# Kernel optimization log

Measured on AMD Instinct MI355X. Metric: run time of the kernel, lower is better.

Reference implementation:

```python
import jax, jax.numpy as jnp
import numpy as np

T, B, DIM_IN, DIM_STATE, NUM_CLASSES = 256, 64, 256, 512, 10000


def setup_inputs() -> dict:
    key = jax.random.key(0)
    ks = jax.random.split(key, 6)
    inputs = jax.random.normal(ks[0], (T, B, DIM_IN), dtype=jnp.float32)
    labels = jax.random.uniform(ks[1], (T, B, NUM_CLASSES), dtype=jnp.float32)
    labels = labels / jnp.sum(labels, axis=-1, keepdims=True)  # soft label distributions
    initial_state = jnp.zeros((B, DIM_STATE), dtype=jnp.float32)
    initial_output = jnp.zeros((B, DIM_STATE), dtype=jnp.float32)
    # LSTM cell params: gates packed as [i, f, g, o]
    Wx = jax.random.normal(ks[2], (DIM_IN, 4 * DIM_STATE), dtype=jnp.float32) * (1.0 / np.sqrt(DIM_IN))
    Wh = jax.random.normal(ks[3], (DIM_STATE, 4 * DIM_STATE), dtype=jnp.float32) * (1.0 / np.sqrt(DIM_STATE))
    b = jnp.zeros((4 * DIM_STATE,), dtype=jnp.float32)
    # Final FC (softmax head) params
    Wo = jax.random.normal(ks[4], (DIM_STATE, NUM_CLASSES), dtype=jnp.float32) * (1.0 / np.sqrt(DIM_STATE))
    bo = jnp.zeros((NUM_CLASSES,), dtype=jnp.float32)
    return {"inputs": inputs, "labels": labels, "initial_state": initial_state,
            "initial_output": initial_output, "Wx": Wx, "Wh": Wh, "b": b, "Wo": Wo, "bo": bo}


def reference(inputs, labels, initial_state, initial_output, Wx, Wh, b, Wo, bo):
    def step(carry, x_t):
        h, c = carry  # h: [B, DIM_STATE] previous output; c: [B, DIM_STATE] cell state
        z = x_t @ Wx + h @ Wh + b  # [B, 4*DIM_STATE]
        i, f, g, o = jnp.split(z, 4, axis=-1)
        c = jax.nn.sigmoid(f) * c + jax.nn.sigmoid(i) * jnp.tanh(g)
        h = jax.nn.sigmoid(o) * jnp.tanh(c)
        return (h, c), h

    _, hs = jax.lax.scan(step, (initial_output, initial_state), inputs)  # hs: [T, B, DIM_STATE]
    logits = jnp.einsum('tbs,sc->tbc', hs, Wo) + bo  # [T, B, NUM_CLASSES]
    log_p = jax.nn.log_softmax(logits, axis=-1)
    predictions = jnp.exp(log_p)  # softmax probabilities
    # softmax_cross_entropy_with_logits per (t, b), then mean over all
    total_loss = -jnp.mean(jnp.sum(labels * log_p, axis=-1))
    return predictions, total_loss
```

## Files before the change

kernel.cpp:

```cpp
#include <hip/hip_runtime.h>
#include <hip/hip_bf16.h>
#include <math.h>

#define T_STEPS 256
#define BATCH 64
#define DIN 256
#define DSTATE 512
#define NGATE 2048
#define NCLS 10000
#define NCLS_PAD 10112
#define ROWS 16384
#define SCAN_BLOCKS 64
#define GROUP_BLOCKS 16
#define CHUNK_ROWS 4096

typedef __attribute__((ext_vector_type(8))) short bf16x8;
typedef __attribute__((ext_vector_type(4))) float f32x4;

__device__ inline unsigned short f2b(float x) {
    __hip_bfloat16 h = __float2bfloat16(x);
    return *(unsigned short*)&h;
}
__device__ inline float b2f(unsigned short u) {
    return __uint_as_float(((unsigned int)u) << 16);
}

__launch_bounds__(256)
__global__ void prep_all(const float* __restrict__ inputs, const float* __restrict__ Wx,
                         const float* __restrict__ Wh, const float* __restrict__ bias,
                         const float* __restrict__ h0, const float* __restrict__ Wo,
                         unsigned short* __restrict__ Xb, unsigned short* __restrict__ WxT,
                         unsigned short* __restrict__ WhT, float* __restrict__ bp,
                         unsigned short* __restrict__ h0b, unsigned* __restrict__ bar,
                         unsigned short* __restrict__ WoT) {
    __shared__ float tile[64][65];
    const int bid = blockIdx.x;
    const int tid = threadIdx.x;
    if (bid < 4096) {
        int i = bid * 256 + tid;
        float4 v = *(const float4*)&inputs[(size_t)i * 4];
        ushort4 o; o.x = f2b(v.x); o.y = f2b(v.y); o.z = f2b(v.z); o.w = f2b(v.w);
        *(ushort4*)&Xb[(size_t)i * 4] = o;
    } else if (bid < 8192) {
        int e = (bid - 4096) * 256 + tid;
        int jp = e >> 9, k = e & 511;
        int s = jp >> 2, g = jp & 3;
        WhT[e] = f2b(Wh[(size_t)k * NGATE + g * DSTATE + s]);
    } else if (bid < 10240) {
        int e = (bid - 8192) * 256 + tid;
        int jp = e >> 8, k = e & 255;
        int s = jp >> 2, g = jp & 3;
        WxT[e] = f2b(Wx[(size_t)k * NGATE + g * DSTATE + s]);
    } else if (bid < 10248) {
        int jp = (bid - 10240) * 256 + tid;
        if (jp < NGATE) bp[jp] = bias[(jp & 3) * DSTATE + (jp >> 2)];
    } else if (bid < 10280) {
        int i = (bid - 10248) * 256 + tid;
        if (i < BATCH * DSTATE / 4) {
            float4 v = *(const float4*)&h0[(size_t)i * 4];
            ushort4 o; o.x = f2b(v.x); o.y = f2b(v.y); o.z = f2b(v.z); o.w = f2b(v.w);
            *(ushort4*)&h0b[(size_t)i * 4] = o;
        }
    } else if (bid < 10284) {
        bar[(bid - 10280) * 256 + tid] = 0u;
    } else {
        int nb = bid - 10284;
        int n0 = (nb % 158) * 64, k0 = (nb / 158) * 64;
        #pragma unroll
        for (int r = 0; r < 16; ++r) {
            int k = (tid >> 6) + r * 4;
            int n = tid & 63;
            float v = (n0 + n < NCLS) ? Wo[(size_t)(k0 + k) * NCLS + n0 + n] : 0.f;
            tile[k][n] = v;
        }
        __syncthreads();
        #pragma unroll
        for (int r = 0; r < 16; ++r) {
            int n = (tid >> 6) + r * 4;
            int k = tid & 63;
            WoT[(size_t)(n0 + n) * DSTATE + k0 + k] = f2b(tile[k][n]);
        }
    }
}

__launch_bounds__(256)
__global__ void zx_gemm(const unsigned short* __restrict__ Xb,
                        const unsigned short* __restrict__ WxT,
                        const float* __restrict__ bp,
                        unsigned short* __restrict__ ZxT) {
    __shared__ unsigned short As[64][264];
    __shared__ unsigned short Bs[128][264];
    __shared__ float zls[4][32][65];
    const int tid = threadIdx.x;
    const int t = blockIdx.x;
    const int n0 = blockIdx.y * 128;
    const int wave = tid >> 6, lane = tid & 63, mr = lane & 15, g = lane >> 4;

    #pragma unroll
    for (int r = 0; r < 8; ++r) {
        int c = r * 256 + tid; int row = c >> 5, q = c & 31;
        *(int4*)&As[row][q * 8] = *(const int4*)&Xb[((size_t)t * 64 + row) * DIN + q * 8];
    }
    #pragma unroll
    for (int r = 0; r < 16; ++r) {
        int c = r * 256 + tid; int row = c >> 5, q = c & 31;
        *(int4*)&Bs[row][q * 8] = *(const int4*)&WxT[(size_t)(n0 + row) * DIN + q * 8];
    }
    __syncthreads();

    f32x4 acc[4][2] = {};
    #pragma unroll
    for (int kt = 0; kt < DIN; kt += 32) {
        bf16x8 af[4], bf[2];
        #pragma unroll
        for (int fm = 0; fm < 4; ++fm) af[fm] = *(const bf16x8*)&As[fm * 16 + mr][kt + g * 8];
        #pragma unroll
        for (int fn = 0; fn < 2; ++fn) bf[fn] = *(const bf16x8*)&Bs[wave * 32 + fn * 16 + mr][kt + g * 8];
        #pragma unroll
        for (int fm = 0; fm < 4; ++fm)
            #pragma unroll
            for (int fn = 0; fn < 2; ++fn)
                acc[fm][fn] = __builtin_amdgcn_mfma_f32_16x16x32_bf16(af[fm], bf[fn], acc[fm][fn], 0, 0, 0);
    }
    #pragma unroll
    for (int fm = 0; fm < 4; ++fm)
        #pragma unroll
        for (int fn = 0; fn < 2; ++fn)
            #pragma unroll
            for (int r = 0; r < 4; ++r)
                zls[wave][fn * 16 + mr][fm * 16 + g * 4 + r] = acc[fm][fn][r];
    #pragma unroll 4
    for (int jr = 0; jr < 32; ++jr) {
        int j = n0 + wave * 32 + jr;
        float v = zls[wave][jr][lane] + bp[j];
        ZxT[((size_t)t * NGATE + j) * 64 + lane] = f2b(v);
    }
}

__device__ __forceinline__ void groupbar(unsigned* fbase, int w, unsigned want, int tid) {
    __syncthreads();
    if (tid == 0)
        __hip_atomic_store(&fbase[w * 16], want, __ATOMIC_RELEASE, __HIP_MEMORY_SCOPE_AGENT);
    if (tid < GROUP_BLOCKS) {
        while (__hip_atomic_load(&fbase[tid * 16], __ATOMIC_RELAXED, __HIP_MEMORY_SCOPE_AGENT) < want) {}
        (void)__hip_atomic_load(&fbase[tid * 16], __ATOMIC_ACQUIRE, __HIP_MEMORY_SCOPE_AGENT);
    }
    __syncthreads();
}

__launch_bounds__(256, 1)
__global__ void lstm_scan_mfma(const unsigned short* __restrict__ h0b,
                               const float* __restrict__ c0,
                               const unsigned short* __restrict__ WhT,
                               const unsigned short* __restrict__ ZxT,
                               unsigned short* __restrict__ hsb,
                               unsigned* __restrict__ bar) {
    __shared__ unsigned short Wl[128][520];
    __shared__ unsigned short hT[16][520];
    __shared__ float zb[16][132];
    const int tid = threadIdx.x;
    const int bid = blockIdx.x;
    const int grp = bid >> 4;
    const int w   = bid & 15;
    const int b0  = grp * 16;
    const int j0  = w * 128;
    const int s0  = w * 32;
    const int wave = tid >> 6, lane = tid & 63, mr = lane & 15, gl = lane >> 4;
    unsigned* fbase = bar + grp * 256;

    #pragma unroll 4
    for (int r = 0; r < 32; ++r) {
        int c = r * 256 + tid; int row = c >> 6, q = c & 63;
        *(int4*)&Wl[row][q * 8] = *(const int4*)&WhT[(size_t)(j0 + row) * DSTATE + q * 8];
    }

    const int gb  = lane >> 2;
    const int slg = wave * 8 + (lane & 3) * 2;
    float creg0 = c0[(b0 + gb) * DSTATE + s0 + slg];
    float creg1 = c0[(b0 + gb) * DSTATE + s0 + slg + 1];
    __syncthreads();

    const size_t zo0 = ((size_t)(j0 + wave * 32 + mr)) * 64 + b0 + gl * 4;
    const size_t zo1 = ((size_t)(j0 + wave * 32 + 16 + mr)) * 64 + b0 + gl * 4;
    ushort4 za0 = *(const ushort4*)&ZxT[zo0];
    ushort4 za1 = *(const ushort4*)&ZxT[zo1];

    for (int t = 0; t < T_STEPS; ++t) {
        const unsigned short* hsrc = t ? (hsb + (size_t)(t - 1) * BATCH * DSTATE) : h0b;
        #pragma unroll
        for (int r = 0; r < 4; ++r) {
            int c = r * 256 + tid; int row = c >> 6, q = c & 63;
            *(int4*)&hT[row][q * 8] = *(const int4*)&hsrc[(size_t)(b0 + row) * DSTATE + q * 8];
        }
        __syncthreads();

        f32x4 acc0, acc1;
        acc0[0] = b2f(za0.x); acc0[1] = b2f(za0.y); acc0[2] = b2f(za0.z); acc0[3] = b2f(za0.w);
        acc1[0] = b2f(za1.x); acc1[1] = b2f(za1.y); acc1[2] = b2f(za1.z); acc1[3] = b2f(za1.w);
        if (t + 1 < T_STEPS) {
            za0 = *(const ushort4*)&ZxT[(size_t)(t + 1) * NGATE * 64 + zo0];
            za1 = *(const ushort4*)&ZxT[(size_t)(t + 1) * NGATE * 64 + zo1];
        }
        #pragma unroll
        for (int kt = 0; kt < DSTATE; kt += 32) {
            bf16x8 af = *(const bf16x8*)&hT[mr][kt + gl * 8];
            acc0 = __builtin_amdgcn_mfma_f32_16x16x32_bf16(af, *(const bf16x8*)&Wl[wave * 32 + mr][kt + gl * 8], acc0, 0, 0, 0);
            acc1 = __builtin_amdgcn_mfma_f32_16x16x32_bf16(af, *(const bf16x8*)&Wl[wave * 32 + 16 + mr][kt + gl * 8], acc1, 0, 0, 0);
        }
        #pragma unroll
        for (int r = 0; r < 4; ++r) {
            zb[gl * 4 + r][wave * 32 + mr] = acc0[r];
            zb[gl * 4 + r][wave * 32 + 16 + mr] = acc1[r];
        }
        {
            float zi0 = zb[gb][slg * 4 + 0], zf0 = zb[gb][slg * 4 + 1];
            float zg0 = zb[gb][slg * 4 + 2], zo0v = zb[gb][slg * 4 + 3];
            float zi1 = zb[gb][slg * 4 + 4], zf1 = zb[gb][slg * 4 + 5];
            float zg1 = zb[gb][slg * 4 + 6], zo1v = zb[gb][slg * 4 + 7];
            float i0 = 1.f / (1.f + expf(-zi0)), f0 = 1.f / (1.f + expf(-zf0));
            float o0 = 1.f / (1.f + expf(-zo0v)), g0 = tanhf(zg0);
            float i1 = 1.f / (1.f + expf(-zi1)), f1 = 1.f / (1.f + expf(-zf1));
            float o1 = 1.f / (1.f + expf(-zo1v)), g1 = tanhf(zg1);
            creg0 = f0 * creg0 + i0 * g0;
            creg1 = f1 * creg1 + i1 * g1;
            float h0v = o0 * tanhf(creg0);
            float h1v = o1 * tanhf(creg1);
            ushort2 hv; hv.x = f2b(h0v); hv.y = f2b(h1v);
            *(ushort2*)&hsb[((size_t)t * BATCH + b0 + gb) * DSTATE + s0 + slg] = hv;
        }
        if (t != T_STEPS - 1)
            groupbar(fbase, w, (unsigned)(t + 1), tid);
    }
}

__launch_bounds__(256)
__global__ void gemm_logits_bf16(const unsigned short* __restrict__ A,
                                 const unsigned short* __restrict__ Bt,
                                 const float* __restrict__ bo,
                                 unsigned short* __restrict__ Cb) {
    __shared__ unsigned short As[128 * 32];
    __shared__ unsigned short Bs[128 * 32];
    __shared__ unsigned short sC[128][136];
    const int tid = threadIdx.x;
    const int wave = tid >> 6, lane = tid & 63;
    const int wm = wave >> 1, wn = wave & 1;
    const int m0 = blockIdx.y * 128, n0 = blockIdx.x * 128;
    const int g = lane >> 4, mr = lane & 15;

    const int ch0 = wave * 64 + lane;
    const int ch1 = (4 + wave) * 64 + lane;
    const int row0 = ch0 >> 2, q0 = ch0 & 3;
    const int row1 = ch1 >> 2, q1 = ch1 & 3;

    f32x4 acc[4][4] = {};
    for (int kt = 0; kt < DSTATE; kt += 32) {
        __builtin_amdgcn_global_load_lds(
            (const __attribute__((address_space(1))) void*)&A[(size_t)(m0 + row0) * DSTATE + kt + q0 * 8],
            (__attribute__((address_space(3))) void*)&As[ch0 * 8 - lane * 8], 16, 0, 0);
        __builtin_amdgcn_global_load_lds(
            (const __attribute__((address_space(1))) void*)&A[(size_t)(m0 + row1) * DSTATE + kt + q1 * 8],
            (__attribute__((address_space(3))) void*)&As[ch1 * 8 - lane * 8], 16, 0, 0);
        __builtin_amdgcn_global_load_lds(
            (const __attribute__((address_space(1))) void*)&Bt[(size_t)(n0 + row0) * DSTATE + kt + q0 * 8],
            (__attribute__((address_space(3))) void*)&Bs[ch0 * 8 - lane * 8], 16, 0, 0);
        __builtin_amdgcn_global_load_lds(
            (const __attribute__((address_space(1))) void*)&Bt[(size_t)(n0 + row1) * DSTATE + kt + q1 * 8],
            (__attribute__((address_space(3))) void*)&Bs[ch1 * 8 - lane * 8], 16, 0, 0);
        __syncthreads();

        bf16x8 af[4], bf[4];
        #pragma unroll
        for (int f = 0; f < 4; ++f) {
            af[f] = *(const bf16x8*)&As[(wm * 64 + f * 16 + mr) * 32 + g * 8];
            bf[f] = *(const bf16x8*)&Bs[(wn * 64 + f * 16 + mr) * 32 + g * 8];
        }
        #pragma unroll
        for (int fm = 0; fm < 4; ++fm)
            #pragma unroll
            for (int fn = 0; fn < 4; ++fn)
                acc[fm][fn] = __builtin_amdgcn_mfma_f32_16x16x32_bf16(af[fm], bf[fn], acc[fm][fn], 0, 0, 0);
        __syncthreads();
    }
    #pragma unroll
    for (int fn = 0; fn < 4; ++fn) {
        int colg = n0 + wn * 64 + fn * 16 + mr;
        float bias = (colg < NCLS) ? bo[colg] : 0.f;
        #pragma unroll
        for (int fm = 0; fm < 4; ++fm)
            #pragma unroll
            for (int r = 0; r < 4; ++r)
                sC[wm * 64 + fm * 16 + g * 4 + r][wn * 64 + fn * 16 + mr] = f2b(acc[fm][fn][r] + bias);
    }
    __syncthreads();
    #pragma unroll
    for (int rr = 0; rr < 8; ++rr) {
        int row_l = (tid >> 4) + rr * 16;
        int col0 = (tid & 15) * 8;
        int gcol = n0 + col0;
        if (gcol < NCLS)
            *(int4*)&Cb[(size_t)(m0 + row_l) * NCLS + gcol] = *(int4*)&sC[row_l][col0];
    }
}

__launch_bounds__(256)
__global__ void gemm_logits_mfma(const unsigned short* __restrict__ A,
                                 const unsigned short* __restrict__ Bt,
                                 const float* __restrict__ bo,
                                 float* __restrict__ C) {
    __shared__ unsigned short As[128 * 32];
    __shared__ unsigned short Bs[128 * 32];
    const int tid = threadIdx.x;
    const int wave = tid >> 6, lane = tid & 63;
    const int wm = wave >> 1, wn = wave & 1;
    const int m0 = blockIdx.y * 128, n0 = blockIdx.x * 128;
    const int g = lane >> 4, mr = lane & 15;

    const int ch0 = wave * 64 + lane;
    const int ch1 = (4 + wave) * 64 + lane;
    const int row0 = ch0 >> 2, q0 = ch0 & 3;
    const int row1 = ch1 >> 2, q1 = ch1 & 3;

    f32x4 acc[4][4] = {};
    for (int kt = 0; kt < DSTATE; kt += 32) {
        __builtin_amdgcn_global_load_lds(
            (const __attribute__((address_space(1))) void*)&A[(size_t)(m0 + row0) * DSTATE + kt + q0 * 8],
            (__attribute__((address_space(3))) void*)&As[ch0 * 8 - lane * 8], 16, 0, 0);
        __builtin_amdgcn_global_load_lds(
            (const __attribute__((address_space(1))) void*)&A[(size_t)(m0 + row1) * DSTATE + kt + q1 * 8],
            (__attribute__((address_space(3))) void*)&As[ch1 * 8 - lane * 8], 16, 0, 0);
        __builtin_amdgcn_global_load_lds(
            (const __attribute__((address_space(1))) void*)&Bt[(size_t)(n0 + row0) * DSTATE + kt + q0 * 8],
            (__attribute__((address_space(3))) void*)&Bs[ch0 * 8 - lane * 8], 16, 0, 0);
        __builtin_amdgcn_global_load_lds(
            (const __attribute__((address_space(1))) void*)&Bt[(size_t)(n0 + row1) * DSTATE + kt + q1 * 8],
            (__attribute__((address_space(3))) void*)&Bs[ch1 * 8 - lane * 8], 16, 0, 0);
        __syncthreads();

        bf16x8 af[4], bf[4];
        #pragma unroll
        for (int f = 0; f < 4; ++f) {
            af[f] = *(const bf16x8*)&As[(wm * 64 + f * 16 + mr) * 32 + g * 8];
            bf[f] = *(const bf16x8*)&Bs[(wn * 64 + f * 16 + mr) * 32 + g * 8];
        }
        #pragma unroll
        for (int fm = 0; fm < 4; ++fm)
            #pragma unroll
            for (int fn = 0; fn < 4; ++fn)
                acc[fm][fn] = __builtin_amdgcn_mfma_f32_16x16x32_bf16(af[fm], bf[fn], acc[fm][fn], 0, 0, 0);
        __syncthreads();
    }
    #pragma unroll
    for (int fm = 0; fm < 4; ++fm) {
        #pragma unroll
        for (int fn = 0; fn < 4; ++fn) {
            int col = n0 + wn * 64 + fn * 16 + mr;
            if (col >= NCLS) continue;
            float bias = bo[col];
            #pragma unroll
            for (int r = 0; r < 4; ++r) {
                int row = m0 + wm * 64 + fm * 16 + g * 4 + r;
                C[(size_t)row * NCLS + col] = acc[fm][fn][r] + bias;
            }
        }
    }
}

__device__ inline float wave_reduce_max(float v) {
    #pragma unroll
    for (int off = 32; off > 0; off >>= 1) v = fmaxf(v, __shfl_xor(v, off));
    return v;
}
__device__ inline float wave_reduce_sum(float v) {
    #pragma unroll
    for (int off = 32; off > 0; off >>= 1) v += __shfl_xor(v, off);
    return v;
}

__launch_bounds__(512)
__global__ void softmax_loss_bf16(const unsigned short* __restrict__ Cb,
                                  const float* __restrict__ labels,
                                  float* __restrict__ probs,
                                  float* __restrict__ rowloss) {
    __shared__ float row[NCLS];
    __shared__ float sm[8];
    const int tid = threadIdx.x;
    const size_t base = (size_t)blockIdx.x * NCLS;

    float m = -INFINITY;
    for (int c8 = tid; c8 < NCLS / 8; c8 += 512) {
        ushort4 u0 = *(const ushort4*)&Cb[base + c8 * 8];
        ushort4 u1 = *(const ushort4*)&Cb[base + c8 * 8 + 4];
        float v0 = b2f(u0.x), v1 = b2f(u0.y), v2 = b2f(u0.z), v3 = b2f(u0.w);
        float v4 = b2f(u1.x), v5 = b2f(u1.y), v6 = b2f(u1.z), v7 = b2f(u1.w);
        float4 a = {v0, v1, v2, v3}, b = {v4, v5, v6, v7};
        *(float4*)&row[c8 * 8] = a;
        *(float4*)&row[c8 * 8 + 4] = b;
        m = fmaxf(m, fmaxf(fmaxf(fmaxf(v0, v1), fmaxf(v2, v3)),
                           fmaxf(fmaxf(v4, v5), fmaxf(v6, v7))));
    }
    m = wave_reduce_max(m);
    if ((tid & 63) == 0) sm[tid >> 6] = m;
    __syncthreads();
    m = fmaxf(fmaxf(fmaxf(sm[0], sm[1]), fmaxf(sm[2], sm[3])),
              fmaxf(fmaxf(sm[4], sm[5]), fmaxf(sm[6], sm[7])));
    __syncthreads();

    float s = 0.f, dot = 0.f;
    for (int c4 = tid; c4 < NCLS / 4; c4 += 512) {
        float4 v = *(const float4*)&row[c4 * 4];
        float4 lb = *(const float4*)&labels[base + c4 * 4];
        s += expf(v.x - m) + expf(v.y - m) + expf(v.z - m) + expf(v.w - m);
        dot += lb.x * v.x + lb.y * v.y + lb.z * v.z + lb.w * v.w;
    }
    s = wave_reduce_sum(s);
    if ((tid & 63) == 0) sm[tid >> 6] = s;
    __syncthreads();
    s = ((sm[0] + sm[1]) + (sm[2] + sm[3])) + ((sm[4] + sm[5]) + (sm[6] + sm[7]));
    __syncthreads();
    dot = wave_reduce_sum(dot);
    if ((tid & 63) == 0) sm[tid >> 6] = dot;
    __syncthreads();
    dot = ((sm[0] + sm[1]) + (sm[2] + sm[3])) + ((sm[4] + sm[5]) + (sm[6] + sm[7]));

    float inv = 1.f / s;
    for (int c4 = tid; c4 < NCLS / 4; c4 += 512) {
        float4 v = *(const float4*)&row[c4 * 4];
        float4 o;
        o.x = expf(v.x - m) * inv; o.y = expf(v.y - m) * inv;
        o.z = expf(v.z - m) * inv; o.w = expf(v.w - m) * inv;
        *(float4*)&probs[base + c4 * 4] = o;
    }
    if (tid == 0) rowloss[blockIdx.x] = (m + logf(s)) - dot;
}

__launch_bounds__(256)
__global__ void softmax_loss(float* __restrict__ logits,
                             const float* __restrict__ labels,
                             float* __restrict__ rowloss) {
    __shared__ float row[NCLS];
    __shared__ float sm[4];
    const int tid = threadIdx.x;
    const size_t base = (size_t)blockIdx.x * NCLS;

    float m = -INFINITY;
    for (int c4 = tid; c4 < NCLS / 4; c4 += 256) {
        float4 v = *(const float4*)&logits[base + c4 * 4];
        *(float4*)&row[c4 * 4] = v;
        m = fmaxf(fmaxf(m, fmaxf(v.x, v.y)), fmaxf(v.z, v.w));
    }
    m = wave_reduce_max(m);
    if ((tid & 63) == 0) sm[tid >> 6] = m;
    __syncthreads();
    m = fmaxf(fmaxf(sm[0], sm[1]), fmaxf(sm[2], sm[3]));
    __syncthreads();

    float s = 0.f, dot = 0.f;
    for (int c4 = tid; c4 < NCLS / 4; c4 += 256) {
        float4 v = *(const float4*)&row[c4 * 4];
        float4 lb = *(const float4*)&labels[base + c4 * 4];
        s += expf(v.x - m) + expf(v.y - m) + expf(v.z - m) + expf(v.w - m);
        dot += lb.x * v.x + lb.y * v.y + lb.z * v.z + lb.w * v.w;
    }
    s = wave_reduce_sum(s);
    if ((tid & 63) == 0) sm[tid >> 6] = s;
    __syncthreads();
    s = sm[0] + sm[1] + sm[2] + sm[3];
    __syncthreads();
    dot = wave_reduce_sum(dot);
    if ((tid & 63) == 0) sm[tid >> 6] = dot;
    __syncthreads();
    dot = sm[0] + sm[1] + sm[2] + sm[3];

    float inv = 1.f / s;
    for (int c4 = tid; c4 < NCLS / 4; c4 += 256) {
        float4 v = *(const float4*)&row[c4 * 4];
        float4 o;
        o.x = expf(v.x - m) * inv; o.y = expf(v.y - m) * inv;
        o.z = expf(v.z - m) * inv; o.w = expf(v.w - m) * inv;
        *(float4*)&logits[base + c4 * 4] = o;
    }
    if (tid == 0) rowloss[blockIdx.x] = (m + logf(s)) - dot;
}

__launch_bounds__(256)
__global__ void loss_reduce(const float* __restrict__ rowloss, float* __restrict__ out) {
    __shared__ float sm[4];
    float s = 0.f;
    for (int i = threadIdx.x; i < ROWS; i += 256) s += rowloss[i];
    s = wave_reduce_sum(s);
    if ((threadIdx.x & 63) == 0) sm[threadIdx.x >> 6] = s;
    __syncthreads();
    if (threadIdx.x == 0) out[0] = (sm[0] + sm[1] + sm[2] + sm[3]) * (1.f / ROWS);
}

extern "C" void kernel_launch(void* const* d_in, const int* in_sizes, int n_in,
                              void* d_out, int out_size, void* d_ws, size_t ws_size,
                              hipStream_t stream) {
    const float* inputs = (const float*)d_in[0];
    const float* labels = (const float*)d_in[1];
    const float* c0     = (const float*)d_in[2];
    const float* h0     = (const float*)d_in[3];
    const float* Wx     = (const float*)d_in[4];
    const float* Wh     = (const float*)d_in[5];
    const float* bias   = (const float*)d_in[6];
    const float* Wo     = (const float*)d_in[7];
    const float* bo     = (const float*)d_in[8];
    float* out = (float*)d_out;

    float* ws = (float*)d_ws;
    float* bp       = ws;
    float* rowloss  = bp + 2048;
    unsigned short* WhT = (unsigned short*)(rowloss + 16384);
    unsigned short* WxT = WhT + 1048576;
    unsigned short* Xb  = WxT + 524288;
    unsigned short* h0b = Xb + 4194304;
    unsigned short* hsb = h0b + 32768;
    unsigned short* WoT = hsb + 8388608;
    unsigned short* ZxT = WoT + 5177344;
    unsigned* bar = (unsigned*)(ZxT + 33554432);
    unsigned short* Cb = (unsigned short*)(bar + 1024);

    size_t base_bytes = (size_t)((char*)Cb - (char*)d_ws);
    size_t need_bf16 = base_bytes + (size_t)CHUNK_ROWS * NCLS * sizeof(unsigned short);
    bool use_bf16 = (ws_size >= need_bf16);

    prep_all<<<11548, 256, 0, stream>>>(inputs, Wx, Wh, bias, h0, Wo,
                                        Xb, WxT, WhT, bp, h0b, bar, WoT);

    zx_gemm<<<dim3(T_STEPS, NGATE / 128), 256, 0, stream>>>(Xb, WxT, bp, ZxT);

    void* args[] = {(void*)&h0b, (void*)&c0, (void*)&WhT, (void*)&ZxT, (void*)&hsb, (void*)&bar};
    hipLaunchCooperativeKernel((const void*)lstm_scan_mfma, dim3(SCAN_BLOCKS), dim3(256),
                               args, 0, stream);

    if (use_bf16) {
        for (int row0 = 0; row0 < ROWS; row0 += CHUNK_ROWS) {
            gemm_logits_bf16<<<dim3(NCLS_PAD / 128, CHUNK_ROWS / 128), 256, 0, stream>>>(
                hsb + (size_t)row0 * DSTATE, WoT, bo, Cb);
            softmax_loss_bf16<<<CHUNK_ROWS, 512, 0, stream>>>(
                Cb, labels + (size_t)row0 * NCLS, out + (size_t)row0 * NCLS, rowloss + row0);
        }
    } else {
        gemm_logits_mfma<<<dim3(NCLS_PAD / 128, ROWS / 128), 256, 0, stream>>>(hsb, WoT, bo, out);
        softmax_loss<<<ROWS, 256, 0, stream>>>(out, labels, rowloss);
    }
    loss_reduce<<<1, 256, 0, stream>>>(rowloss, out + (size_t)ROWS * NCLS);
}
```

Before: 1.893 ms.

## Fuse LSTM scan with chunked logits GEMM and softmax in one cooperative kernel

Replaces the separate scan, per-chunk logits GEMM and softmax launches with one cooperative mega-kernel. 64 blocks run the recurrence while 192 worker blocks wait on per-block progress flags and compute logits and softmax/loss for each 64-timestep chunk as soon as it is ready. The aim is to overlap the serial scan with the output head and remove launch gaps. In exchange, the scan blocks now run at 512 threads with half of them idle, the worker blocks spin-wait, and the workers also need grid-wide barriers between GEMM and softmax phases. Because the Cb buffer is shared across chunks, later chunks cannot start until the previous chunk's softmax has finished.

```diff
diff --git a/kernel.cpp b/kernel.cpp
--- a/kernel.cpp
+++ b/kernel.cpp
@@ -9,9 +9,11 @@
 #define NGATE 2048
 #define NCLS 10000
 #define NCLS_PAD 10112
+#define NCLS_PAD2 10240
 #define ROWS 16384
 #define SCAN_BLOCKS 64
 #define GROUP_BLOCKS 16
+#define WORK_BLK 192
 #define CHUNK_ROWS 4096
 
 typedef __attribute__((ext_vector_type(8))) short bf16x8;
@@ -61,11 +63,11 @@
             ushort4 o; o.x = f2b(v.x); o.y = f2b(v.y); o.z = f2b(v.z); o.w = f2b(v.w);
             *(ushort4*)&h0b[(size_t)i * 4] = o;
         }
-    } else if (bid < 10284) {
+    } else if (bid < 10296) {
         bar[(bid - 10280) * 256 + tid] = 0u;
     } else {
-        int nb = bid - 10284;
-        int n0 = (nb % 158) * 64, k0 = (nb / 158) * 64;
+        int nb = bid - 10296;
+        int n0 = (nb % 160) * 64, k0 = (nb / 160) * 64;
         #pragma unroll
         for (int r = 0; r < 16; ++r) {
             int k = (tid >> 6) + r * 4;
@@ -148,6 +150,258 @@
     __syncthreads();
 }
 
+__device__ __forceinline__ void workbar(unsigned* wfl, int wid, unsigned want, int tid) {
+    __syncthreads();
+    if (tid == 0)
+        __hip_atomic_store(&wfl[wid * 16], want, __ATOMIC_RELEASE, __HIP_MEMORY_SCOPE_AGENT);
+    if (tid < WORK_BLK) {
+        while (__hip_atomic_load(&wfl[tid * 16], __ATOMIC_RELAXED, __HIP_MEMORY_SCOPE_AGENT) < want)
+            __builtin_amdgcn_s_sleep(1);
+        (void)__hip_atomic_load(&wfl[tid * 16], __ATOMIC_ACQUIRE, __HIP_MEMORY_SCOPE_AGENT);
+    }
+    __syncthreads();
+}
+
+__device__ inline float wave_reduce_max(float v) {
+    #pragma unroll
+    for (int off = 32; off > 0; off >>= 1) v = fmaxf(v, __shfl_xor(v, off));
+    return v;
+}
+__device__ inline float wave_reduce_sum(float v) {
+    #pragma unroll
+    for (int off = 32; off > 0; off >>= 1) v += __shfl_xor(v, off);
+    return v;
+}
+
+__launch_bounds__(512, 1)
+__global__ void lstm_mega(const unsigned short* __restrict__ h0b,
+                          const float* __restrict__ c0,
+                          const unsigned short* __restrict__ WhT,
+                          const unsigned short* __restrict__ ZxT,
+                          unsigned short* __restrict__ hsb,
+                          unsigned* __restrict__ bar,
+                          const unsigned short* __restrict__ WoT,
+                          const float* __restrict__ bo,
+                          const float* __restrict__ labels,
+                          unsigned short* __restrict__ Cb,
+                          float* __restrict__ probs,
+                          float* __restrict__ rowloss) {
+    __shared__ __align__(16) char smem[158208];
+    const int tid = threadIdx.x;
+    const int bid = blockIdx.x;
+
+    if (bid < SCAN_BLOCKS) {
+        unsigned short (*Wl)[520] = (unsigned short(*)[520])smem;
+        unsigned short (*hT)[520] = (unsigned short(*)[520])(smem + 133120);
+        float (*zb)[132] = (float(*)[132])(smem + 149760);
+        const int grp = bid >> 4, w = bid & 15;
+        const int b0 = grp * 16, j0 = w * 128, s0 = w * 32;
+        const int wave = tid >> 6, lane = tid & 63, mr = lane & 15, gl = lane >> 4;
+        unsigned* fbase = bar + grp * 256;
+
+        if (tid < 256) {
+            #pragma unroll 4
+            for (int r = 0; r < 32; ++r) {
+                int c = r * 256 + tid; int row = c >> 6, q = c & 63;
+                *(int4*)&Wl[row][q * 8] = *(const int4*)&WhT[(size_t)(j0 + row) * DSTATE + q * 8];
+            }
+        }
+        const int gb  = lane >> 2;
+        const int slg = wave * 8 + (lane & 3) * 2;
+        float creg0 = 0.f, creg1 = 0.f;
+        if (tid < 256) {
+            creg0 = c0[(b0 + gb) * DSTATE + s0 + slg];
+            creg1 = c0[(b0 + gb) * DSTATE + s0 + slg + 1];
+        }
+        __syncthreads();
+
+        size_t zo0 = 0, zo1 = 0;
+        ushort4 za0 = {0,0,0,0}, za1 = {0,0,0,0};
+        if (tid < 256) {
+            zo0 = ((size_t)(j0 + wave * 32 + mr)) * 64 + b0 + gl * 4;
+            zo1 = ((size_t)(j0 + wave * 32 + 16 + mr)) * 64 + b0 + gl * 4;
+            za0 = *(const ushort4*)&ZxT[zo0];
+            za1 = *(const ushort4*)&ZxT[zo1];
+        }
+
+        for (int t = 0; t < T_STEPS; ++t) {
+            const unsigned short* hsrc = t ? (hsb + (size_t)(t - 1) * BATCH * DSTATE) : h0b;
+            if (tid < 256) {
+                #pragma unroll
+                for (int r = 0; r < 4; ++r) {
+                    int c = r * 256 + tid; int row = c >> 6, q = c & 63;
+                    *(int4*)&hT[row][q * 8] = *(const int4*)&hsrc[(size_t)(b0 + row) * DSTATE + q * 8];
+                }
+            }
+            __syncthreads();
+            if (tid < 256) {
+                f32x4 acc0, acc1;
+                acc0[0] = b2f(za0.x); acc0[1] = b2f(za0.y); acc0[2] = b2f(za0.z); acc0[3] = b2f(za0.w);
+                acc1[0] = b2f(za1.x); acc1[1] = b2f(za1.y); acc1[2] = b2f(za1.z); acc1[3] = b2f(za1.w);
+                if (t + 1 < T_STEPS) {
+                    za0 = *(const ushort4*)&ZxT[(size_t)(t + 1) * NGATE * 64 + zo0];
+                    za1 = *(const ushort4*)&ZxT[(size_t)(t + 1) * NGATE * 64 + zo1];
+                }
+                #pragma unroll
+                for (int kt = 0; kt < DSTATE; kt += 32) {
+                    bf16x8 af = *(const bf16x8*)&hT[mr][kt + gl * 8];
+                    acc0 = __builtin_amdgcn_mfma_f32_16x16x32_bf16(af, *(const bf16x8*)&Wl[wave * 32 + mr][kt + gl * 8], acc0, 0, 0, 0);
+                    acc1 = __builtin_amdgcn_mfma_f32_16x16x32_bf16(af, *(const bf16x8*)&Wl[wave * 32 + 16 + mr][kt + gl * 8], acc1, 0, 0, 0);
+                }
+                #pragma unroll
+                for (int r = 0; r < 4; ++r) {
+                    zb[gl * 4 + r][wave * 32 + mr] = acc0[r];
+                    zb[gl * 4 + r][wave * 32 + 16 + mr] = acc1[r];
+                }
+                float zi0 = zb[gb][slg * 4 + 0], zf0 = zb[gb][slg * 4 + 1];
+                float zg0 = zb[gb][slg * 4 + 2], zo0v = zb[gb][slg * 4 + 3];
+                float zi1 = zb[gb][slg * 4 + 4], zf1 = zb[gb][slg * 4 + 5];
+                float zg1 = zb[gb][slg * 4 + 6], zo1v = zb[gb][slg * 4 + 7];
+                float i0 = 1.f / (1.f + expf(-zi0)), f0 = 1.f / (1.f + expf(-zf0));
+                float o0 = 1.f / (1.f + expf(-zo0v)), g0 = tanhf(zg0);
+                float i1 = 1.f / (1.f + expf(-zi1)), f1 = 1.f / (1.f + expf(-zf1));
+                float o1 = 1.f / (1.f + expf(-zo1v)), g1 = tanhf(zg1);
+                creg0 = f0 * creg0 + i0 * g0;
+                creg1 = f1 * creg1 + i1 * g1;
+                float h0v = o0 * tanhf(creg0);
+                float h1v = o1 * tanhf(creg1);
+                ushort2 hv; hv.x = f2b(h0v); hv.y = f2b(h1v);
+                *(ushort2*)&hsb[((size_t)t * BATCH + b0 + gb) * DSTATE + s0 + slg] = hv;
+            }
+            if (t != T_STEPS - 1)
+                groupbar(fbase, w, (unsigned)(t + 1), tid);
+        }
+        __syncthreads();
+        if (tid == 0)
+            __hip_atomic_store(&fbase[w * 16], (unsigned)T_STEPS, __ATOMIC_RELEASE, __HIP_MEMORY_SCOPE_AGENT);
+        return;
+    }
+
+    const int wid = bid - SCAN_BLOCKS;
+    unsigned* wfl = bar + 1024;
+    unsigned short* As = (unsigned short*)smem;
+    unsigned short* Bs = (unsigned short*)(smem + 8192);
+    unsigned short (*sC)[264] = (unsigned short(*)[264])(smem + 24576);
+    float* rowf = (float*)smem;
+    float* smr  = (float*)(smem + 40000);
+    const int wave = tid >> 6, lane = tid & 63, mr = lane & 15, g = lane >> 4;
+    const int wm = wave >> 2, wn = wave & 3;
+
+    for (int c4 = 0; c4 < 4; ++c4) {
+        unsigned target = (c4 < 3) ? 64u * (c4 + 1) : (unsigned)T_STEPS;
+        if (tid < 64) {
+            unsigned* f = &bar[(tid >> 4) * 256 + (tid & 15) * 16];
+            while (__hip_atomic_load(f, __ATOMIC_RELAXED, __HIP_MEMORY_SCOPE_AGENT) < target)
+                __builtin_amdgcn_s_sleep(8);
+            (void)__hip_atomic_load(f, __ATOMIC_ACQUIRE, __HIP_MEMORY_SCOPE_AGENT);
+        }
+        __syncthreads();
+        const unsigned short* A = hsb + (size_t)c4 * CHUNK_ROWS * DSTATE;
+
+        for (int tile = wid; tile < 32 * 40; tile += WORK_BLK) {
+            const int m0 = (tile & 31) * 128;
+            const int n0 = (tile >> 5) * 256;
+            f32x4 acc[4][4] = {};
+            for (int kt = 0; kt < DSTATE; kt += 32) {
+                __builtin_amdgcn_global_load_lds(
+                    (const __attribute__((address_space(1))) void*)&A[(size_t)(m0 + (tid >> 2)) * DSTATE + kt + (tid & 3) * 8],
+                    (__attribute__((address_space(3))) void*)&As[tid * 8 - lane * 8], 16, 0, 0);
+                __builtin_amdgcn_global_load_lds(
+                    (const __attribute__((address_space(1))) void*)&WoT[(size_t)(n0 + (tid >> 2)) * DSTATE + kt + (tid & 3) * 8],
+                    (__attribute__((address_space(3))) void*)&Bs[tid * 8 - lane * 8], 16, 0, 0);
+                __builtin_amdgcn_global_load_lds(
+                    (const __attribute__((address_space(1))) void*)&WoT[(size_t)(n0 + 128 + (tid >> 2)) * DSTATE + kt + (tid & 3) * 8],
+                    (__attribute__((address_space(3))) void*)&Bs[4096 + tid * 8 - lane * 8], 16, 0, 0);
+                __syncthreads();
+                bf16x8 af[4], bf[4];
+                #pragma unroll
+                for (int f = 0; f < 4; ++f) {
+                    af[f] = *(const bf16x8*)&As[(wm * 64 + f * 16 + mr) * 32 + g * 8];
+                    bf[f] = *(const bf16x8*)&Bs[(wn * 64 + f * 16 + mr) * 32 + g * 8];
+                }
+                #pragma unroll
+                for (int fm = 0; fm < 4; ++fm)
+                    #pragma unroll
+                    for (int fn = 0; fn < 4; ++fn)
+                        acc[fm][fn] = __builtin_amdgcn_mfma_f32_16x16x32_bf16(af[fm], bf[fn], acc[fm][fn], 0, 0, 0);
+                __syncthreads();
+            }
+            #pragma unroll
+            for (int fn = 0; fn < 4; ++fn) {
+                int colg = n0 + wn * 64 + fn * 16 + mr;
+                float bias = (colg < NCLS) ? bo[colg] : 0.f;
+                #pragma unroll
+                for (int fm = 0; fm < 4; ++fm)
+                    #pragma unroll
+                    for (int r = 0; r < 4; ++r)
+                        sC[wm * 64 + fm * 16 + g * 4 + r][wn * 64 + fn * 16 + mr] = f2b(acc[fm][fn][r] + bias);
+            }
+            __syncthreads();
+            #pragma unroll
+            for (int rr = 0; rr < 8; ++rr) {
+                int row_l = (tid >> 5) + rr * 16;
+                int col0 = (tid & 31) * 8;
+                if (n0 + col0 < NCLS)
+                    *(int4*)&Cb[(size_t)(m0 + row_l) * NCLS + n0 + col0] = *(int4*)&sC[row_l][col0];
+            }
+            __syncthreads();
+        }
+        workbar(wfl, wid, (unsigned)(2 * c4 + 1), tid);
+
+        for (int r = wid; r < CHUNK_ROWS; r += WORK_BLK) {
+            const size_t cbase = (size_t)r * NCLS;
+            const size_t gbase = ((size_t)c4 * CHUNK_ROWS + r) * NCLS;
+            float m = -INFINITY;
+            for (int c8 = tid; c8 < NCLS / 8; c8 += 512) {
+                ushort4 u0 = *(const ushort4*)&Cb[cbase + c8 * 8];
+                ushort4 u1 = *(const ushort4*)&Cb[cbase + c8 * 8 + 4];
+                float v0 = b2f(u0.x), v1 = b2f(u0.y), v2 = b2f(u0.z), v3 = b2f(u0.w);
+                float v4 = b2f(u1.x), v5 = b2f(u1.y), v6 = b2f(u1.z), v7 = b2f(u1.w);
+                float4 a = {v0, v1, v2, v3}, b = {v4, v5, v6, v7};
+                *(float4*)&rowf[c8 * 8] = a;
+                *(float4*)&rowf[c8 * 8 + 4] = b;
+                m = fmaxf(m, fmaxf(fmaxf(fmaxf(v0, v1), fmaxf(v2, v3)),
+                                   fmaxf(fmaxf(v4, v5), fmaxf(v6, v7))));
+            }
+            m = wave_reduce_max(m);
+            if ((tid & 63) == 0) smr[tid >> 6] = m;
+            __syncthreads();
+            m = fmaxf(fmaxf(fmaxf(smr[0], smr[1]), fmaxf(smr[2], smr[3])),
+                      fmaxf(fmaxf(smr[4], smr[5]), fmaxf(smr[6], smr[7])));
+            __syncthreads();
+
+            float s = 0.f, dot = 0.f;
+            for (int q = tid; q < NCLS / 4; q += 512) {
+                float4 v = *(const float4*)&rowf[q * 4];
+                float4 lb = *(const float4*)&labels[gbase + q * 4];
+                s += expf(v.x - m) + expf(v.y - m) + expf(v.z - m) + expf(v.w - m);
+                dot += lb.x * v.x + lb.y * v.y + lb.z * v.z + lb.w * v.w;
+            }
+            s = wave_reduce_sum(s);
+            if ((tid & 63) == 0) smr[tid >> 6] = s;
+            __syncthreads();
+            s = ((smr[0] + smr[1]) + (smr[2] + smr[3])) + ((smr[4] + smr[5]) + (smr[6] + smr[7]));
+            __syncthreads();
+            dot = wave_reduce_sum(dot);
+            if ((tid & 63) == 0) smr[tid >> 6] = dot;
+            __syncthreads();
+            dot = ((smr[0] + smr[1]) + (smr[2] + smr[3])) + ((smr[4] + smr[5]) + (smr[6] + smr[7]));
+
+            float inv = 1.f / s;
+            for (int q = tid; q < NCLS / 4; q += 512) {
+                float4 v = *(const float4*)&rowf[q * 4];
+                float4 o;
+                o.x = expf(v.x - m) * inv; o.y = expf(v.y - m) * inv;
+                o.z = expf(v.z - m) * inv; o.w = expf(v.w - m) * inv;
+                *(float4*)&probs[gbase + q * 4] = o;
+            }
+            if (tid == 0) rowloss[c4 * CHUNK_ROWS + r] = (m + logf(s)) - dot;
+            __syncthreads();
+        }
+        if (c4 < 3) workbar(wfl, wid, (unsigned)(2 * c4 + 2), tid);
+    }
+}
+
 __launch_bounds__(256, 1)
 __global__ void lstm_scan_mfma(const unsigned short* __restrict__ h0b,
                                const float* __restrict__ c0,
@@ -160,11 +414,8 @@
     __shared__ float zb[16][132];
     const int tid = threadIdx.x;
     const int bid = blockIdx.x;
-    const int grp = bid >> 4;
-    const int w   = bid & 15;
-    const int b0  = grp * 16;
-    const int j0  = w * 128;
-    const int s0  = w * 32;
+    const int grp = bid >> 4, w = bid & 15;
+    const int b0 = grp * 16, j0 = w * 128, s0 = w * 32;
     const int wave = tid >> 6, lane = tid & 63, mr = lane & 15, gl = lane >> 4;
     unsigned* fbase = bar + grp * 256;
 
@@ -173,8 +424,7 @@
         int c = r * 256 + tid; int row = c >> 6, q = c & 63;
         *(int4*)&Wl[row][q * 8] = *(const int4*)&WhT[(size_t)(j0 + row) * DSTATE + q * 8];
     }
-
-    const int gb  = lane >> 2;
+    const int gb = lane >> 2;
     const int slg = wave * 8 + (lane & 3) * 2;
     float creg0 = c0[(b0 + gb) * DSTATE + s0 + slg];
     float creg1 = c0[(b0 + gb) * DSTATE + s0 + slg + 1];
@@ -193,7 +443,6 @@
             *(int4*)&hT[row][q * 8] = *(const int4*)&hsrc[(size_t)(b0 + row) * DSTATE + q * 8];
         }
         __syncthreads();
-
         f32x4 acc0, acc1;
         acc0[0] = b2f(za0.x); acc0[1] = b2f(za0.y); acc0[2] = b2f(za0.z); acc0[3] = b2f(za0.w);
         acc1[0] = b2f(za1.x); acc1[1] = b2f(za1.y); acc1[2] = b2f(za1.z); acc1[3] = b2f(za1.w);
@@ -234,19 +483,17 @@
 }
 
 __launch_bounds__(256)
-__global__ void gemm_logits_bf16(const unsigned short* __restrict__ A,
+__global__ void gemm_logits_mfma(const unsigned short* __restrict__ A,
                                  const unsigned short* __restrict__ Bt,
                                  const float* __restrict__ bo,
-                                 unsigned short* __restrict__ Cb) {
+                                 float* __restrict__ C) {
     __shared__ unsigned short As[128 * 32];
     __shared__ unsigned short Bs[128 * 32];
-    __shared__ unsigned short sC[128][136];
     const int tid = threadIdx.x;
     const int wave = tid >> 6, lane = tid & 63;
     const int wm = wave >> 1, wn = wave & 1;
     const int m0 = blockIdx.y * 128, n0 = blockIdx.x * 128;
     const int g = lane >> 4, mr = lane & 15;
-
     const int ch0 = wave * 64 + lane;
     const int ch1 = (4 + wave) * 64 + lane;
     const int row0 = ch0 >> 2, q0 = ch0 & 3;
@@ -267,75 +514,6 @@
             (const __attribute__((address_space(1))) void*)&Bt[(size_t)(n0 + row1) * DSTATE + kt + q1 * 8],
             (__attribute__((address_space(3))) void*)&Bs[ch1 * 8 - lane * 8], 16, 0, 0);
         __syncthreads();
-
-        bf16x8 af[4], bf[4];
-        #pragma unroll
-        for (int f = 0; f < 4; ++f) {
-            af[f] = *(const bf16x8*)&As[(wm * 64 + f * 16 + mr) * 32 + g * 8];
-            bf[f] = *(const bf16x8*)&Bs[(wn * 64 + f * 16 + mr) * 32 + g * 8];
-        }
-        #pragma unroll
-        for (int fm = 0; fm < 4; ++fm)
-            #pragma unroll
-            for (int fn = 0; fn < 4; ++fn)
-                acc[fm][fn] = __builtin_amdgcn_mfma_f32_16x16x32_bf16(af[fm], bf[fn], acc[fm][fn], 0, 0, 0);
-        __syncthreads();
-    }
-    #pragma unroll
-    for (int fn = 0; fn < 4; ++fn) {
-        int colg = n0 + wn * 64 + fn * 16 + mr;
-        float bias = (colg < NCLS) ? bo[colg] : 0.f;
-        #pragma unroll
-        for (int fm = 0; fm < 4; ++fm)
-            #pragma unroll
-            for (int r = 0; r < 4; ++r)
-                sC[wm * 64 + fm * 16 + g * 4 + r][wn * 64 + fn * 16 + mr] = f2b(acc[fm][fn][r] + bias);
-    }
-    __syncthreads();
-    #pragma unroll
-    for (int rr = 0; rr < 8; ++rr) {
-        int row_l = (tid >> 4) + rr * 16;
-        int col0 = (tid & 15) * 8;
-        int gcol = n0 + col0;
-        if (gcol < NCLS)
-            *(int4*)&Cb[(size_t)(m0 + row_l) * NCLS + gcol] = *(int4*)&sC[row_l][col0];
-    }
-}
-
-__launch_bounds__(256)
-__global__ void gemm_logits_mfma(const unsigned short* __restrict__ A,
-                                 const unsigned short* __restrict__ Bt,
-                                 const float* __restrict__ bo,
-                                 float* __restrict__ C) {
-    __shared__ unsigned short As[128 * 32];
-    __shared__ unsigned short Bs[128 * 32];
-    const int tid = threadIdx.x;
-    const int wave = tid >> 6, lane = tid & 63;
-    const int wm = wave >> 1, wn = wave & 1;
-    const int m0 = blockIdx.y * 128, n0 = blockIdx.x * 128;
-    const int g = lane >> 4, mr = lane & 15;
-
-    const int ch0 = wave * 64 + lane;
-    const int ch1 = (4 + wave) * 64 + lane;
-    const int row0 = ch0 >> 2, q0 = ch0 & 3;
-    const int row1 = ch1 >> 2, q1 = ch1 & 3;
-
-    f32x4 acc[4][4] = {};
-    for (int kt = 0; kt < DSTATE; kt += 32) {
-        __builtin_amdgcn_global_load_lds(
-            (const __attribute__((address_space(1))) void*)&A[(size_t)(m0 + row0) * DSTATE + kt + q0 * 8],
-            (__attribute__((address_space(3))) void*)&As[ch0 * 8 - lane * 8], 16, 0, 0);
-        __builtin_amdgcn_global_load_lds(
-            (const __attribute__((address_space(1))) void*)&A[(size_t)(m0 + row1) * DSTATE + kt + q1 * 8],
-            (__attribute__((address_space(3))) void*)&As[ch1 * 8 - lane * 8], 16, 0, 0);
-        __builtin_amdgcn_global_load_lds(
-            (const __attribute__((address_space(1))) void*)&Bt[(size_t)(n0 + row0) * DSTATE + kt + q0 * 8],
-            (__attribute__((address_space(3))) void*)&Bs[ch0 * 8 - lane * 8], 16, 0, 0);
-        __builtin_amdgcn_global_load_lds(
-            (const __attribute__((address_space(1))) void*)&Bt[(size_t)(n0 + row1) * DSTATE + kt + q1 * 8],
-            (__attribute__((address_space(3))) void*)&Bs[ch1 * 8 - lane * 8], 16, 0, 0);
-        __syncthreads();
-
         bf16x8 af[4], bf[4];
         #pragma unroll
         for (int f = 0; f < 4; ++f) {
@@ -363,74 +541,6 @@
             }
         }
     }
-}
-
-__device__ inline float wave_reduce_max(float v) {
-    #pragma unroll
-    for (int off = 32; off > 0; off >>= 1) v = fmaxf(v, __shfl_xor(v, off));
-    return v;
-}
-__device__ inline float wave_reduce_sum(float v) {
-    #pragma unroll
-    for (int off = 32; off > 0; off >>= 1) v += __shfl_xor(v, off);
-    return v;
-}
-
-__launch_bounds__(512)
-__global__ void softmax_loss_bf16(const unsigned short* __restrict__ Cb,
-                                  const float* __restrict__ labels,
-                                  float* __restrict__ probs,
-                                  float* __restrict__ rowloss) {
-    __shared__ float row[NCLS];
-    __shared__ float sm[8];
-    const int tid = threadIdx.x;
-    const size_t base = (size_t)blockIdx.x * NCLS;
-
-    float m = -INFINITY;
-    for (int c8 = tid; c8 < NCLS / 8; c8 += 512) {
-        ushort4 u0 = *(const ushort4*)&Cb[base + c8 * 8];
-        ushort4 u1 = *(const ushort4*)&Cb[base + c8 * 8 + 4];
-        float v0 = b2f(u0.x), v1 = b2f(u0.y), v2 = b2f(u0.z), v3 = b2f(u0.w);
-        float v4 = b2f(u1.x), v5 = b2f(u1.y), v6 = b2f(u1.z), v7 = b2f(u1.w);
-        float4 a = {v0, v1, v2, v3}, b = {v4, v5, v6, v7};
-        *(float4*)&row[c8 * 8] = a;
-        *(float4*)&row[c8 * 8 + 4] = b;
-        m = fmaxf(m, fmaxf(fmaxf(fmaxf(v0, v1), fmaxf(v2, v3)),
-                           fmaxf(fmaxf(v4, v5), fmaxf(v6, v7))));
-    }
-    m = wave_reduce_max(m);
-    if ((tid & 63) == 0) sm[tid >> 6] = m;
-    __syncthreads();
-    m = fmaxf(fmaxf(fmaxf(sm[0], sm[1]), fmaxf(sm[2], sm[3])),
-              fmaxf(fmaxf(sm[4], sm[5]), fmaxf(sm[6], sm[7])));
-    __syncthreads();
-
-    float s = 0.f, dot = 0.f;
-    for (int c4 = tid; c4 < NCLS / 4; c4 += 512) {
-        float4 v = *(const float4*)&row[c4 * 4];
-        float4 lb = *(const float4*)&labels[base + c4 * 4];
-        s += expf(v.x - m) + expf(v.y - m) + expf(v.z - m) + expf(v.w - m);
-        dot += lb.x * v.x + lb.y * v.y + lb.z * v.z + lb.w * v.w;
-    }
-    s = wave_reduce_sum(s);
-    if ((tid & 63) == 0) sm[tid >> 6] = s;
-    __syncthreads();
-    s = ((sm[0] + sm[1]) + (sm[2] + sm[3])) + ((sm[4] + sm[5]) + (sm[6] + sm[7]));
-    __syncthreads();
-    dot = wave_reduce_sum(dot);
-    if ((tid & 63) == 0) sm[tid >> 6] = dot;
-    __syncthreads();
-    dot = ((sm[0] + sm[1]) + (sm[2] + sm[3])) + ((sm[4] + sm[5]) + (sm[6] + sm[7]));
-
-    float inv = 1.f / s;
-    for (int c4 = tid; c4 < NCLS / 4; c4 += 512) {
-        float4 v = *(const float4*)&row[c4 * 4];
-        float4 o;
-        o.x = expf(v.x - m) * inv; o.y = expf(v.y - m) * inv;
-        o.z = expf(v.z - m) * inv; o.w = expf(v.w - m) * inv;
-        *(float4*)&probs[base + c4 * 4] = o;
-    }
-    if (tid == 0) rowloss[blockIdx.x] = (m + logf(s)) - dot;
 }
 
 __launch_bounds__(256)
@@ -516,31 +626,29 @@
     unsigned short* h0b = Xb + 4194304;
     unsigned short* hsb = h0b + 32768;
     unsigned short* WoT = hsb + 8388608;
-    unsigned short* ZxT = WoT + 5177344;
+    unsigned short* ZxT = WoT + 5242880;
     unsigned* bar = (unsigned*)(ZxT + 33554432);
-    unsigned short* Cb = (unsigned short*)(bar + 1024);
+    unsigned short* Cb = (unsigned short*)(bar + 4096);
 
     size_t base_bytes = (size_t)((char*)Cb - (char*)d_ws);
-    size_t need_bf16 = base_bytes + (size_t)CHUNK_ROWS * NCLS * sizeof(unsigned short);
-    bool use_bf16 = (ws_size >= need_bf16);
-
-    prep_all<<<11548, 256, 0, stream>>>(inputs, Wx, Wh, bias, h0, Wo,
+    size_t need_fused = base_bytes + (size_t)CHUNK_ROWS * NCLS * sizeof(unsigned short);
+    bool use_fused = (ws_size >= need_fused);
+
+    prep_all<<<11576, 256, 0, stream>>>(inputs, Wx, Wh, bias, h0, Wo,
                                         Xb, WxT, WhT, bp, h0b, bar, WoT);
 
     zx_gemm<<<dim3(T_STEPS, NGATE / 128), 256, 0, stream>>>(Xb, WxT, bp, ZxT);
 
-    void* args[] = {(void*)&h0b, (void*)&c0, (void*)&WhT, (void*)&ZxT, (void*)&hsb, (void*)&bar};
-    hipLaunchCooperativeKernel((const void*)lstm_scan_mfma, dim3(SCAN_BLOCKS), dim3(256),
-                               args, 0, stream);
-
-    if (use_bf16) {
-        for (int row0 = 0; row0 < ROWS; row0 += CHUNK_ROWS) {
-            gemm_logits_bf16<<<dim3(NCLS_PAD / 128, CHUNK_ROWS / 128), 256, 0, stream>>>(
-                hsb + (size_t)row0 * DSTATE, WoT, bo, Cb);
-            softmax_loss_bf16<<<CHUNK_ROWS, 512, 0, stream>>>(
-                Cb, labels + (size_t)row0 * NCLS, out + (size_t)row0 * NCLS, rowloss + row0);
-        }
+    if (use_fused) {
+        void* args[] = {(void*)&h0b, (void*)&c0, (void*)&WhT, (void*)&ZxT, (void*)&hsb,
+                        (void*)&bar, (void*)&WoT, (void*)&bo, (void*)&labels,
+                        (void*)&Cb, (void*)&out, (void*)&rowloss};
+        hipLaunchCooperativeKernel((const void*)lstm_mega, dim3(SCAN_BLOCKS + WORK_BLK),
+                                   dim3(512), args, 0, stream);
     } else {
+        void* args[] = {(void*)&h0b, (void*)&c0, (void*)&WhT, (void*)&ZxT, (void*)&hsb, (void*)&bar};
+        hipLaunchCooperativeKernel((const void*)lstm_scan_mfma, dim3(SCAN_BLOCKS),
+                                   dim3(256), args, 0, stream);
         gemm_logits_mfma<<<dim3(NCLS_PAD / 128, ROWS / 128), 256, 0, stream>>>(hsb, WoT, bo, out);
         softmax_loss<<<ROWS, 256, 0, stream>>>(out, labels, rowloss);
     }
```

Measured after the change: 1.982 ms. 1.05x slower.
